# Performance work log

Measured on AMD Instinct MI355X. Metric: run time of the kernel, lower is better.

Reference implementation:

```python
import jax, jax.numpy as jnp
from jax import lax
import numpy as np

B = 2048
N = 10  # wires on q_device0
C64 = jnp.complex64

# fixed gate matrices (qubit ordering matches wire-list order)
S_ = jnp.array([[1, 0], [0, 1j]], C64)
T_ = jnp.array([[1, 0], [0, np.exp(1j * np.pi / 4)]], C64)
SX_ = 0.5 * jnp.array([[1 + 1j, 1 - 1j], [1 - 1j, 1 + 1j]], C64)
Y_ = jnp.array([[0, -1j], [1j, 0]], C64)
CNOT_ = jnp.array([[1, 0, 0, 0], [0, 1, 0, 0], [0, 0, 0, 1], [0, 0, 1, 0]], C64)
CZ_ = jnp.diag(jnp.array([1, 1, 1, -1], C64))
CY_ = jnp.array([[1, 0, 0, 0], [0, 1, 0, 0], [0, 0, 0, -1j], [0, 0, 1j, 0]], C64)
SWAP_ = jnp.array([[1, 0, 0, 0], [0, 0, 1, 0], [0, 1, 0, 0], [0, 0, 0, 1]], C64)
_cs = np.eye(8); _cs[[5, 6]] = _cs[[6, 5]]  # CSWAP: |101> <-> |110>
CSWAP_ = jnp.array(_cs, C64)
_tf = np.eye(8); _tf[[6, 7]] = _tf[[7, 6]]  # Toffoli: |110> <-> |111>
TOFF_ = jnp.array(_tf, C64)

# parametrized single-qubit gate builders; t scalar -> [2,2], t [B] -> [B,2,2]
def _rx(t):
    c = jnp.cos(t / 2).astype(C64)
    s = -1j * jnp.sin(t / 2).astype(C64)
    return jnp.stack([jnp.stack([c, s], -1), jnp.stack([s, c], -1)], -2)

def _ry(t):
    c = jnp.cos(t / 2).astype(C64)
    s = jnp.sin(t / 2).astype(C64)
    return jnp.stack([jnp.stack([c, -s], -1), jnp.stack([s, c], -1)], -2)

def _rz(t):
    a = jnp.exp(-0.5j * t.astype(C64))
    b = jnp.exp(0.5j * t.astype(C64))
    z = jnp.zeros_like(a)
    return jnp.stack([jnp.stack([a, z], -1), jnp.stack([z, b], -1)], -2)

def _phase(t):
    e = jnp.exp(1j * t.astype(C64))
    o = jnp.ones_like(e)
    z = jnp.zeros_like(e)
    return jnp.stack([jnp.stack([o, z], -1), jnp.stack([z, e], -1)], -2)

def _rot(phi, th, om):  # RZ(om) RY(th) RZ(phi), pennylane/torchquantum convention
    c = jnp.cos(th / 2).astype(C64)
    s = jnp.sin(th / 2).astype(C64)
    p = phi.astype(C64); w = om.astype(C64)
    m00 = jnp.exp(-0.5j * (p + w)) * c
    m01 = -jnp.exp(0.5j * (p - w)) * s
    m10 = jnp.exp(-0.5j * (p - w)) * s
    m11 = jnp.exp(0.5j * (p + w)) * c
    return jnp.stack([jnp.stack([m00, m01], -1), jnp.stack([m10, m11], -1)], -2)

def _apply1(psi, U, w):  # psi: [B]+(2,)*N, U: [2,2] or [B,2,2]
    s = jnp.moveaxis(psi, w + 1, 1)
    if U.ndim == 2:
        s = jnp.einsum('ij,bj...->bi...', U, s)
    else:
        s = jnp.einsum('bij,bj...->bi...', U, s)
    return jnp.moveaxis(s, 1, w + 1)

def _applyk(psi, U, wires):  # fixed k-qubit gate, U: [2^k, 2^k]
    k = len(wires)
    axes = tuple(w + 1 for w in wires)
    s = jnp.moveaxis(psi, axes, tuple(range(1, k + 1)))
    sh = s.shape
    s = s.reshape((sh[0], 2 ** k) + sh[k + 1:])
    s = jnp.einsum('ij,bj...->bi...', U, s)
    return jnp.moveaxis(s.reshape(sh), tuple(range(1, k + 1)), axes)

def _forward(x, conv1_w, conv1_b, conv2_w, conv2_b, fc1_w, fc1_b, fc2_w, fc2_b,
             theta0, theta_rz, theta_ps, rot_p):
    dn = ('NCHW', 'OIHW', 'NCHW')
    h = lax.conv_general_dilated(x, conv1_w, (1, 1), 'VALID', dimension_numbers=dn)
    h = jax.nn.relu(h + conv1_b[None, :, None, None])
    h = lax.conv_general_dilated(h, conv2_w, (1, 1), 'VALID', dimension_numbers=dn)
    h = jax.nn.relu(h + conv2_b[None, :, None, None])
    h = lax.reduce_window(h, -jnp.inf, lax.max, (1, 1, 2, 2), (1, 1, 2, 2), 'VALID')
    h = h.reshape(h.shape[0], -1)  # [B, 9216], dropout = identity (eval)
    h = jax.nn.relu(h @ fc1_w.T + fc1_b)
    a = jax.nn.sigmoid(h @ fc2_w.T + fc2_b) * (2.0 * np.pi)  # angles [B, 10]
    bsz = a.shape[0]
    psi = jnp.zeros((bsz, 2 ** N), C64).at[:, 0].set(1.0).reshape((bsz,) + (2,) * N)
    trz = jnp.reshape(theta_rz, ())
    tps = jnp.reshape(theta_ps, ())
    for k in range(N):                      # TrainableRxAll
        psi = _apply1(psi, _rx(theta0[k]), k)
    for k in range(N):                      # RxAll with input angles
        psi = _apply1(psi, _rx(a[:, k]), k)
    psi = _apply1(psi, _rx(a[:, 1]), 1)
    psi = _apply1(psi, _rx(jnp.asarray(-np.pi / 4, jnp.float32)), 5)  # q_layer2 fixed
    psi = _apply1(psi, _ry(a[:, 2]), 2)
    psi = _apply1(psi, _rz(a[:, 3]), 3)
    psi = _apply1(psi, S_, 4)
    psi = _apply1(psi, T_, 5)
    psi = _apply1(psi, _rz(trz), 6)         # q_layer3
    psi = _apply1(psi, SX_, 7)
    # (q_device1 ops on a separate 3-wire device do not affect the output)
    psi = _applyk(psi, CZ_, (0, 5))
    psi = _applyk(psi, CNOT_, (0, 5))
    psi = _applyk(psi, CY_, (0, 5))
    psi = _applyk(psi, CY_, (3, 8))         # q_layer4
    psi = _applyk(psi, SWAP_, (2, 3))
    psi = _applyk(psi, CSWAP_, (4, 5, 6))
    psi = _applyk(psi, TOFF_, (8, 5, 0))    # q_layer5
    psi = _apply1(psi, _phase(tps), 8)      # q_layer6
    psi = _apply1(psi, _phase(a[:, 7]), 7)
    psi = _apply1(psi, _rot(rot_p[0], rot_p[1], rot_p[2]), 4)  # q_layer7
    psi = _apply1(psi, _rot(a[:, 6], a[:, 7], a[:, 8]), 5)
    axes = tuple(range(1, N + 1))
    evs = [jnp.real(jnp.sum(jnp.conj(psi) * _apply1(psi, Y_, k), axis=axes))
           for k in range(N)]
    ev = jnp.stack(evs, -1)                 # [B, 10] <Y_k>
    return jax.nn.log_softmax(ev, axis=1)


def setup_inputs() -> dict:
    key = jax.random.key(0)
    ks = jax.random.split(key, 13)
    return {
        'x': jax.random.normal(ks[0], (B, 1, 28, 28), jnp.float32),
        'conv1_w': jax.random.normal(ks[1], (32, 1, 3, 3), jnp.float32) * 0.2,
        'conv1_b': jnp.zeros((32,), jnp.float32),
        'conv2_w': jax.random.normal(ks[2], (64, 32, 3, 3), jnp.float32) * 0.05,
        'conv2_b': jnp.zeros((64,), jnp.float32),
        'fc1_w': jax.random.normal(ks[3], (128, 9216), jnp.float32) * 0.01,
        'fc1_b': jnp.zeros((128,), jnp.float32),
        'fc2_w': jax.random.normal(ks[4], (10, 128), jnp.float32) * 0.1,
        'fc2_b': jnp.zeros((10,), jnp.float32),
        'theta0': jax.random.normal(ks[5], (10,), jnp.float32),
        'theta_rz': jax.random.normal(ks[6], (1,), jnp.float32),
        'theta_ps': jax.random.normal(ks[7], (1,), jnp.float32),
        'rot_p': jax.random.normal(ks[8], (3,), jnp.float32),
    }


def reference(x, conv1_w, conv1_b, conv2_w, conv2_b, fc1_w, fc1_b, fc2_w, fc2_b,
              theta0, theta_rz, theta_ps, rot_p):
    return _forward(x, conv1_w, conv1_b, conv2_w, conv2_b, fc1_w, fc1_b, fc2_w, fc2_b,
                    theta0, theta_rz, theta_ps, rot_p)
```

## Files before the change

### kernel.cpp

```cpp
#include <hip/hip_runtime.h>
#include <math.h>

typedef short short8 __attribute__((ext_vector_type(8)));
typedef float f32x4 __attribute__((ext_vector_type(4)));
typedef float f32x16 __attribute__((ext_vector_type(16)));

#define GLB_CP(p) ((const __attribute__((address_space(1))) void*)(p))
#define LDS_CP(p) ((__attribute__((address_space(3))) void*)(p))

__device__ __forceinline__ float2 cmul(float2 a, float2 b) {
    return make_float2(a.x * b.x - a.y * b.y, a.x * b.y + a.y * b.x);
}

__device__ __forceinline__ ushort f2bf(float f) {
    uint u = __float_as_uint(f);
    uint r = (u + 0x7FFFu + ((u >> 16) & 1u)) >> 16;
    return (ushort)r;
}

__global__ __launch_bounds__(256) void prep_kernel(
    const float* __restrict__ c2w, const float* __restrict__ f1w,
    ushort* __restrict__ wt2, ushort* __restrict__ wf1)
{
    int i = blockIdx.x * 256 + threadIdx.x;
    if (i < 18432) {
        int icl = i & 7;
        int t = i >> 3;
        int oc = t & 63;
        int t2 = t >> 6;
        int icg = t2 & 3;
        int tap = t2 >> 2;
        int ic = icg * 8 + icl;
        wt2[i] = f2bf(c2w[(oc * 32 + ic) * 9 + tap]);
    } else if (i < 18432 + 1179648) {
        int j = i - 18432;
        wf1[j] = f2bf(f1w[j]);
    }
}

__global__ __launch_bounds__(256) void conv1_kernel(
    const float* __restrict__ x, const float* __restrict__ w1,
    const float* __restrict__ b1, ushort* __restrict__ h1b)
{
    __shared__ float wl[288];
    __shared__ float bl[32];
    int tid = threadIdx.x;
    for (int e = tid; e < 288; e += 256) wl[e] = w1[e];
    if (tid < 32) bl[tid] = b1[tid];
    __syncthreads();
    int e = blockIdx.x * 256 + tid;
    int icg = e & 3;
    int t = e >> 2;
    int pix = t % 676;
    int b = t / 676;
    int y = pix / 26, xc = pix % 26;
    const float* xp = x + b * 784 + y * 28 + xc;
    float in9[9];
#pragma unroll
    for (int ky = 0; ky < 3; ++ky)
#pragma unroll
        for (int kx = 0; kx < 3; ++kx) in9[ky * 3 + kx] = xp[ky * 28 + kx];
    short8 outv;
#pragma unroll
    for (int o = 0; o < 8; ++o) {
        int oc = icg * 8 + o;
        float acc = bl[oc];
#pragma unroll
        for (int k = 0; k < 9; ++k) acc = fmaf(in9[k], wl[oc * 9 + k], acc);
        outv[o] = (short)f2bf(fmaxf(acc, 0.f));
    }
    *(short8*)&h1b[((b * 4 + icg) * 676 + pix) * 8] = outv;
}

__global__ __launch_bounds__(384, 4) void conv2_banded(
    const ushort* __restrict__ h1b, const ushort* __restrict__ wt2,
    const float* __restrict__ c2b, ushort* __restrict__ pooled)
{
    __shared__ __attribute__((aligned(16))) ushort in_lds[8704];
    __shared__ __attribute__((aligned(16))) ushort wt_lds[16384];
    int bx = blockIdx.x;
    int b = bx / 3;
    int band = bx % 3;
    int r0 = band * 8;
    int tid = threadIdx.x;
    int wave = tid >> 6;
    int lane = tid & 63;
    int lo = lane & 31;
    int hi = lane >> 5;

    for (int c = wave; c < 49; c += 6) {
        if (c < 17) {
            int e = c * 64 + lane;
            if (e > 1039) e = 1039;
            int icg = e / 260;
            int rem = e - icg * 260;
            const ushort* src = h1b + ((size_t)(b * 4 + icg) * 676 + r0 * 26 + rem) * 8;
            __builtin_amdgcn_global_load_lds(GLB_CP(src), LDS_CP(in_lds + c * 512), 16, 0, 0);
        } else {
            int e = (c - 17) * 64 + lane;
            const ushort* src = wt2 + e * 8;
            __builtin_amdgcn_global_load_lds(GLB_CP(src), LDS_CP(wt_lds + (c - 17) * 512), 16, 0, 0);
        }
    }

    short8 w8[2][2];
#pragma unroll
    for (int ks = 0; ks < 2; ++ks)
#pragma unroll
        for (int m = 0; m < 2; ++m)
            w8[ks][m] = *(const short8*)(wt2 + (size_t)((32 + ks * 2 + hi) * 64 + m * 32 + lo) * 8);
    float bias0 = c2b[lo];
    float bias1 = c2b[lo + 32];
    __syncthreads();

    int rx = wave % 3, ry = wave / 3;
    int xcoord = rx * 8 + (lo & 7);
    int ycoord = ry * 4 + (lo >> 3);
    int pbase = ycoord * 26 + xcoord;

    f32x16 acc0 = (f32x16)0.f, acc1 = (f32x16)0.f;

#pragma unroll
    for (int tap = 0; tap < 8; ++tap) {
        int off = (tap / 3) * 26 + (tap % 3);
#pragma unroll
        for (int ks = 0; ks < 2; ++ks) {
            short8 bf = *(const short8*)&in_lds[((ks * 2 + hi) * 260 + pbase + off) * 8];
            short8 a0 = *(const short8*)&wt_lds[((tap * 4 + ks * 2 + hi) * 64 + lo) * 8];
            short8 a1 = *(const short8*)&wt_lds[((tap * 4 + ks * 2 + hi) * 64 + 32 + lo) * 8];
            acc0 = __builtin_amdgcn_mfma_f32_32x32x16_bf16(bf, a0, acc0, 0, 0, 0);
            acc1 = __builtin_amdgcn_mfma_f32_32x32x16_bf16(bf, a1, acc1, 0, 0, 0);
        }
    }
    {
        int off = 2 * 26 + 2;
#pragma unroll
        for (int ks = 0; ks < 2; ++ks) {
            short8 bf = *(const short8*)&in_lds[((ks * 2 + hi) * 260 + pbase + off) * 8];
            acc0 = __builtin_amdgcn_mfma_f32_32x32x16_bf16(bf, w8[ks][0], acc0, 0, 0, 0);
            acc1 = __builtin_amdgcn_mfma_f32_32x32x16_bf16(bf, w8[ks][1], acc1, 0, 0, 0);
        }
    }

    ushort* pout = pooled + (size_t)b * 9216;
    int pcolb = rx * 4 + 2 * hi;
#pragma unroll
    for (int q = 0; q < 2; ++q) {
        int prow = band * 4 + ry * 2 + q;
        int base = 8 * q;
        float m00 = fmaxf(fmaxf(acc0[base], acc0[base + 1]), fmaxf(acc0[base + 4], acc0[base + 5]));
        float m01 = fmaxf(fmaxf(acc0[base + 2], acc0[base + 3]), fmaxf(acc0[base + 6], acc0[base + 7]));
        uint pk0 = (uint)f2bf(fmaxf(m00 + bias0, 0.f)) | ((uint)f2bf(fmaxf(m01 + bias0, 0.f)) << 16);
        *(uint*)&pout[lo * 144 + prow * 12 + pcolb] = pk0;
        float m10 = fmaxf(fmaxf(acc1[base], acc1[base + 1]), fmaxf(acc1[base + 4], acc1[base + 5]));
        float m11 = fmaxf(fmaxf(acc1[base + 2], acc1[base + 3]), fmaxf(acc1[base + 6], acc1[base + 7]));
        uint pk1 = (uint)f2bf(fmaxf(m10 + bias1, 0.f)) | ((uint)f2bf(fmaxf(m11 + bias1, 0.f)) << 16);
        *(uint*)&pout[(lo + 32) * 144 + prow * 12 + pcolb] = pk1;
    }
}

__global__ __launch_bounds__(256) void fc1_mfma(
    const ushort* __restrict__ pooled, const ushort* __restrict__ wf1,
    float* __restrict__ part)
{
    int bx = blockIdx.x, by = blockIdx.y;
    int tid = threadIdx.x;
    int wid = tid >> 6, lane = tid & 63;
    int lo = lane & 15, hi = lane >> 4;
    int m0 = bx * 32;
    int kb = by * 2304;

    f32x4 acc[2][2];
#pragma unroll
    for (int mt = 0; mt < 2; ++mt)
#pragma unroll
        for (int j = 0; j < 2; ++j) acc[mt][j] = (f32x4)0.f;

    const ushort* arow0 = pooled + (size_t)(m0 + lo) * 9216 + kb + hi * 8;
    const ushort* arow1 = arow0 + 16 * 9216;
    const ushort* brow0 = wf1 + (size_t)(wid * 32 + lo) * 9216 + kb + hi * 8;
    const ushort* brow1 = brow0 + 16 * 9216;

    for (int kt = 0; kt < 72; ++kt) {
        short8 a0 = *(const short8*)(arow0 + kt * 32);
        short8 a1 = *(const short8*)(arow1 + kt * 32);
        short8 b0 = *(const short8*)(brow0 + kt * 32);
        short8 b1 = *(const short8*)(brow1 + kt * 32);
        acc[0][0] = __builtin_amdgcn_mfma_f32_16x16x32_bf16(a0, b0, acc[0][0], 0, 0, 0);
        acc[1][0] = __builtin_amdgcn_mfma_f32_16x16x32_bf16(a1, b0, acc[1][0], 0, 0, 0);
        acc[0][1] = __builtin_amdgcn_mfma_f32_16x16x32_bf16(a0, b1, acc[0][1], 0, 0, 0);
        acc[1][1] = __builtin_amdgcn_mfma_f32_16x16x32_bf16(a1, b1, acc[1][1], 0, 0, 0);
    }
    float* pp = part + (size_t)by * 262144;
#pragma unroll
    for (int mt = 0; mt < 2; ++mt)
#pragma unroll
        for (int j = 0; j < 2; ++j)
#pragma unroll
            for (int r = 0; r < 4; ++r)
                pp[(m0 + mt * 16 + hi * 4 + r) * 128 + wid * 32 + j * 16 + lo] = acc[mt][j][r];
}

__global__ __launch_bounds__(256) void fc1_reduce_kernel(
    const float* __restrict__ part, const float* __restrict__ bias,
    float* __restrict__ outp)
{
    int idx = blockIdx.x * 256 + threadIdx.x;
    float s = 0.f;
#pragma unroll
    for (int ks = 0; ks < 4; ++ks) s += part[ks * 262144 + idx];
    outp[idx] = fmaxf(s + bias[idx & 127], 0.f);
}

__global__ __launch_bounds__(256) void fc2_kernel(
    const float* __restrict__ h, const float* __restrict__ w,
    const float* __restrict__ bias, float* __restrict__ ang)
{
    int idx = blockIdx.x * 256 + threadIdx.x;
    if (idx >= 20480) return;
    int b = idx / 10, n = idx % 10;
    const float* hp = h + b * 128;
    const float* wp = w + n * 128;
    float s = bias[n];
    for (int k = 0; k < 128; ++k) s = fmaf(hp[k], wp[k], s);
    ang[idx] = 6.28318530718f / (1.f + expf(-s));
}

__device__ __forceinline__ void apply_rot(float2* s, int p, float phi, float th,
                                          float om, int tid)
{
    float c, sn; sincosf(0.5f * th, &sn, &c);
    float A = 0.5f * (phi + om), Bv = 0.5f * (phi - om);
    float cA, sA; sincosf(A, &sA, &cA);
    float cB, sB; sincosf(Bv, &sB, &cB);
    float2 m00 = make_float2(cA * c, -sA * c);
    float2 m01 = make_float2(-cB * sn, -sB * sn);
    float2 m10 = make_float2(cB * sn, -sB * sn);
    float2 m11 = make_float2(cA * c, sA * c);
    for (int q = tid; q < 512; q += 256) {
        int i0 = ((q >> p) << (p + 1)) | (q & ((1 << p) - 1));
        int i1 = i0 | (1 << p);
        float2 aa = s[i0], bb = s[i1];
        s[i0] = make_float2(m00.x * aa.x - m00.y * aa.y + m01.x * bb.x - m01.y * bb.y,
                            m00.x * aa.y + m00.y * aa.x + m01.x * bb.y + m01.y * bb.x);
        s[i1] = make_float2(m10.x * aa.x - m10.y * aa.y + m11.x * bb.x - m11.y * bb.y,
                            m10.x * aa.y + m10.y * aa.x + m11.x * bb.y + m11.y * bb.x);
    }
}

__global__ __launch_bounds__(256) void quantum_kernel(
    const float* __restrict__ ang, const float* __restrict__ theta0,
    const float* __restrict__ theta_rz, const float* __restrict__ theta_ps,
    const float* __restrict__ rot_p, float* __restrict__ out)
{
    __shared__ float2 s[1024];
    __shared__ float red[40];
    int b = blockIdx.x;
    int tid = threadIdx.x;

    float a[10];
#pragma unroll
    for (int k = 0; k < 10; ++k) a[k] = ang[b * 10 + k];
    float th[10];
#pragma unroll
    for (int k = 0; k < 10; ++k) th[k] = theta0[k] + a[k];
    th[1] += a[1];
    th[5] -= 0.78539816339745f;

    float2 v[10][2];
#pragma unroll
    for (int k = 0; k < 10; ++k) {
        float c, sn; sincosf(0.5f * th[k], &sn, &c);
        v[k][0] = make_float2(c, 0.f);
        v[k][1] = make_float2(0.f, -sn);
    }
    { float c, sn; sincosf(0.5f * a[2], &sn, &c);
      float2 v0 = v[2][0], v1 = v[2][1];
      v[2][0] = make_float2(c * v0.x - sn * v1.x, c * v0.y - sn * v1.y);
      v[2][1] = make_float2(sn * v0.x + c * v1.x, sn * v0.y + c * v1.y); }
    { float c, sn; sincosf(0.5f * a[3], &sn, &c);
      v[3][0] = cmul(v[3][0], make_float2(c, -sn));
      v[3][1] = cmul(v[3][1], make_float2(c, sn)); }
    { float2 t = v[4][1]; v[4][1] = make_float2(-t.y, t.x); }
    { const float r = 0.70710678118655f;
      float2 t = v[5][1]; v[5][1] = make_float2(r * (t.x - t.y), r * (t.x + t.y)); }
    { float c, sn; sincosf(0.5f * theta_rz[0], &sn, &c);
      v[6][0] = cmul(v[6][0], make_float2(c, -sn));
      v[6][1] = cmul(v[6][1], make_float2(c, sn)); }
    { float2 p = v[7][0], q = v[7][1];
      v[7][0] = make_float2(0.5f * ((p.x - p.y) + (q.x + q.y)),
                            0.5f * ((p.x + p.y) + (q.y - q.x)));
      v[7][1] = make_float2(0.5f * ((p.x + p.y) + (q.x - q.y)),
                            0.5f * ((p.y - p.x) + (q.x + q.y))); }

    for (int i = tid; i < 1024; i += 256) {
        float2 c = ((i >> 9) & 1) ? v[0][1] : v[0][0];
#pragma unroll
        for (int k = 1; k < 10; ++k) {
            float2 vk = ((i >> (9 - k)) & 1) ? v[k][1] : v[k][0];
            c = cmul(c, vk);
        }
        s[i] = c;
    }
    __syncthreads();

    for (int i = tid; i < 1024; i += 256)
        if (((i >> 9) & 1) && ((i >> 4) & 1)) { s[i].x = -s[i].x; s[i].y = -s[i].y; }
    __syncthreads();
    { int j = tid;
      int i0 = 512 | ((j >> 4) << 5) | (j & 15);
      int i1 = i0 | 16;
      float2 t0 = s[i0], t1 = s[i1];
      s[i0] = t1; s[i1] = t0; }
    __syncthreads();
    { int j = tid;
      int i0 = 512 | ((j >> 4) << 5) | (j & 15);
      int i1 = i0 | 16;
      float2 t0 = s[i0], t1 = s[i1];
      s[i0] = make_float2(t1.y, -t1.x);
      s[i1] = make_float2(-t0.y, t0.x); }
    __syncthreads();
    { int j = tid;
      int i0 = (j & 1) | (((j >> 1) & 15) << 2) | (((j >> 5) & 7) << 7) | 64;
      int i1 = i0 | 2;
      float2 t0 = s[i0], t1 = s[i1];
      s[i0] = make_float2(t1.y, -t1.x);
      s[i1] = make_float2(-t0.y, t0.x); }
    __syncthreads();
    { int j = tid;
      int i0 = (j & 63) | 128 | (((j >> 6) & 3) << 8);
      int i1 = i0 ^ 0xC0;
      float2 t0 = s[i0], t1 = s[i1];
      s[i0] = t1; s[i1] = t0; }
    __syncthreads();
    if (tid < 128) {
      int j = tid;
      int i0 = (j & 7) | 16 | 32 | (((j >> 3) & 15) << 6);
      int i1 = i0 ^ 0x18;
      float2 t0 = s[i0], t1 = s[i1];
      s[i0] = t1; s[i1] = t0; }
    __syncthreads();
    if (tid < 128) {
      int j = tid;
      int i0 = (j & 1) | 2 | (((j >> 1) & 3) << 2) | 16 | (((j >> 3) & 15) << 5);
      int i1 = i0 | 512;
      float2 t0 = s[i0], t1 = s[i1];
      s[i0] = t1; s[i1] = t0; }
    __syncthreads();
    { float c1, s1; sincosf(theta_ps[0], &s1, &c1);
      float c2, s2; sincosf(a[7], &s2, &c2);
      float2 p1 = make_float2(c1, s1), p2 = make_float2(c2, s2);
      for (int i = tid; i < 1024; i += 256) {
          float2 t = s[i];
          if ((i >> 1) & 1) t = cmul(t, p1);
          if ((i >> 2) & 1) t = cmul(t, p2);
          s[i] = t;
      } }
    __syncthreads();
    apply_rot(s, 5, rot_p[0], rot_p[1], rot_p[2], tid);
    __syncthreads();
    apply_rot(s, 4, a[6], a[7], a[8], tid);
    __syncthreads();

    int wave = tid >> 6;
    for (int k = 0; k < 10; ++k) {
        int p = 9 - k;
        float part = 0.f;
        for (int q = tid; q < 512; q += 256) {
            int i0 = ((q >> p) << (p + 1)) | (q & ((1 << p) - 1));
            int i1 = i0 | (1 << p);
            float2 aa = s[i0], bb = s[i1];
            part += aa.x * bb.y - aa.y * bb.x;
        }
        part *= 2.f;
#pragma unroll
        for (int off = 32; off > 0; off >>= 1)
            part += __shfl_down(part, off, 64);
        if ((tid & 63) == 0) red[k * 4 + wave] = part;
    }
    __syncthreads();
    if (tid == 0) {
        float ev[10];
        float mx = -1e30f;
#pragma unroll
        for (int k = 0; k < 10; ++k) {
            ev[k] = red[k * 4] + red[k * 4 + 1] + red[k * 4 + 2] + red[k * 4 + 3];
            mx = fmaxf(mx, ev[k]);
        }
        float sum = 0.f;
#pragma unroll
        for (int k = 0; k < 10; ++k) sum += expf(ev[k] - mx);
        float lse = mx + logf(sum);
#pragma unroll
        for (int k = 0; k < 10; ++k) out[b * 10 + k] = ev[k] - lse;
    }
}

extern "C" void kernel_launch(void* const* d_in, const int* in_sizes, int n_in,
                              void* d_out, int out_size, void* d_ws, size_t ws_size,
                              hipStream_t stream)
{
    (void)in_sizes; (void)n_in; (void)out_size; (void)ws_size;
    const float* x    = (const float*)d_in[0];
    const float* c1w  = (const float*)d_in[1];
    const float* c1b  = (const float*)d_in[2];
    const float* c2w  = (const float*)d_in[3];
    const float* c2b  = (const float*)d_in[4];
    const float* f1w  = (const float*)d_in[5];
    const float* f1b  = (const float*)d_in[6];
    const float* f2w  = (const float*)d_in[7];
    const float* f2b  = (const float*)d_in[8];
    const float* th0  = (const float*)d_in[9];
    const float* trz  = (const float*)d_in[10];
    const float* tps  = (const float*)d_in[11];
    const float* rotp = (const float*)d_in[12];
    float* out = (float*)d_out;

    char* ws = (char*)d_ws;
    ushort* h1b    = (ushort*)(ws);
    ushort* pooled = (ushort*)(ws + 88604672);
    ushort* wt2    = (ushort*)(ws + 126353408);
    ushort* wf1    = (ushort*)(ws + 126390272);
    float*  part   = (float*)(ws + 128749568);
    float*  fc1o   = (float*)(ws + 132943872);
    float*  ang    = (float*)(ws + 133992448);

    prep_kernel<<<4680, 256, 0, stream>>>(c2w, f1w, wt2, wf1);
    conv1_kernel<<<21632, 256, 0, stream>>>(x, c1w, c1b, h1b);
    conv2_banded<<<6144, 384, 0, stream>>>(h1b, wt2, c2b, pooled);
    fc1_mfma<<<dim3(64, 4), 256, 0, stream>>>(pooled, wf1, part);
    fc1_reduce_kernel<<<1024, 256, 0, stream>>>(part, f1b, fc1o);
    fc2_kernel<<<80, 256, 0, stream>>>(fc1o, f2w, f2b, ang);
    quantum_kernel<<<2048, 256, 0, stream>>>(ang, th0, trz, tps, rotp, out);
}
```

Baseline: 165.8 us.

## Process whole image per conv2 block with double-buffered band prefetch

Result: faster. 161.0 us (-2.9%).

```diff
diff --git a/kernel.cpp b/kernel.cpp
--- a/kernel.cpp
+++ b/kernel.cpp
@@ -72,43 +72,34 @@
     *(short8*)&h1b[((b * 4 + icg) * 676 + pix) * 8] = outv;
 }
 
-__global__ __launch_bounds__(384, 4) void conv2_banded(
+__global__ __launch_bounds__(384, 3) void conv2_img(
     const ushort* __restrict__ h1b, const ushort* __restrict__ wt2,
     const float* __restrict__ c2b, ushort* __restrict__ pooled)
 {
-    __shared__ __attribute__((aligned(16))) ushort in_lds[8704];
-    __shared__ __attribute__((aligned(16))) ushort wt_lds[16384];
-    int bx = blockIdx.x;
-    int b = bx / 3;
-    int band = bx % 3;
-    int r0 = band * 8;
+    __shared__ __attribute__((aligned(16))) ushort wt_lds[18432];
+    __shared__ __attribute__((aligned(16))) ushort in_lds[2][8704];
+    int b = blockIdx.x;
     int tid = threadIdx.x;
     int wave = tid >> 6;
     int lane = tid & 63;
     int lo = lane & 31;
     int hi = lane >> 5;
 
-    for (int c = wave; c < 49; c += 6) {
-        if (c < 17) {
+    for (int c = wave; c < 36; c += 6) {
+        const ushort* src = wt2 + (size_t)(c * 64 + lane) * 8;
+        __builtin_amdgcn_global_load_lds(GLB_CP(src), LDS_CP(wt_lds + c * 512), 16, 0, 0);
+    }
+    {
+        const ushort* base = h1b + (size_t)b * 21632;
+        for (int c = wave; c < 17; c += 6) {
             int e = c * 64 + lane;
             if (e > 1039) e = 1039;
             int icg = e / 260;
             int rem = e - icg * 260;
-            const ushort* src = h1b + ((size_t)(b * 4 + icg) * 676 + r0 * 26 + rem) * 8;
-            __builtin_amdgcn_global_load_lds(GLB_CP(src), LDS_CP(in_lds + c * 512), 16, 0, 0);
-        } else {
-            int e = (c - 17) * 64 + lane;
-            const ushort* src = wt2 + e * 8;
-            __builtin_amdgcn_global_load_lds(GLB_CP(src), LDS_CP(wt_lds + (c - 17) * 512), 16, 0, 0);
-        }
-    }
-
-    short8 w8[2][2];
-#pragma unroll
-    for (int ks = 0; ks < 2; ++ks)
-#pragma unroll
-        for (int m = 0; m < 2; ++m)
-            w8[ks][m] = *(const short8*)(wt2 + (size_t)((32 + ks * 2 + hi) * 64 + m * 32 + lo) * 8);
+            const ushort* src = base + ((size_t)icg * 676 + rem) * 8;
+            __builtin_amdgcn_global_load_lds(GLB_CP(src), LDS_CP(in_lds[0] + c * 512), 16, 0, 0);
+        }
+    }
     float bias0 = c2b[lo];
     float bias1 = c2b[lo + 32];
     __syncthreads();
@@ -117,45 +108,53 @@
     int xcoord = rx * 8 + (lo & 7);
     int ycoord = ry * 4 + (lo >> 3);
     int pbase = ycoord * 26 + xcoord;
-
-    f32x16 acc0 = (f32x16)0.f, acc1 = (f32x16)0.f;
-
-#pragma unroll
-    for (int tap = 0; tap < 8; ++tap) {
-        int off = (tap / 3) * 26 + (tap % 3);
-#pragma unroll
-        for (int ks = 0; ks < 2; ++ks) {
-            short8 bf = *(const short8*)&in_lds[((ks * 2 + hi) * 260 + pbase + off) * 8];
-            short8 a0 = *(const short8*)&wt_lds[((tap * 4 + ks * 2 + hi) * 64 + lo) * 8];
-            short8 a1 = *(const short8*)&wt_lds[((tap * 4 + ks * 2 + hi) * 64 + 32 + lo) * 8];
-            acc0 = __builtin_amdgcn_mfma_f32_32x32x16_bf16(bf, a0, acc0, 0, 0, 0);
-            acc1 = __builtin_amdgcn_mfma_f32_32x32x16_bf16(bf, a1, acc1, 0, 0, 0);
-        }
-    }
-    {
-        int off = 2 * 26 + 2;
-#pragma unroll
-        for (int ks = 0; ks < 2; ++ks) {
-            short8 bf = *(const short8*)&in_lds[((ks * 2 + hi) * 260 + pbase + off) * 8];
-            acc0 = __builtin_amdgcn_mfma_f32_32x32x16_bf16(bf, w8[ks][0], acc0, 0, 0, 0);
-            acc1 = __builtin_amdgcn_mfma_f32_32x32x16_bf16(bf, w8[ks][1], acc1, 0, 0, 0);
-        }
-    }
-
     ushort* pout = pooled + (size_t)b * 9216;
     int pcolb = rx * 4 + 2 * hi;
-#pragma unroll
-    for (int q = 0; q < 2; ++q) {
-        int prow = band * 4 + ry * 2 + q;
-        int base = 8 * q;
-        float m00 = fmaxf(fmaxf(acc0[base], acc0[base + 1]), fmaxf(acc0[base + 4], acc0[base + 5]));
-        float m01 = fmaxf(fmaxf(acc0[base + 2], acc0[base + 3]), fmaxf(acc0[base + 6], acc0[base + 7]));
-        uint pk0 = (uint)f2bf(fmaxf(m00 + bias0, 0.f)) | ((uint)f2bf(fmaxf(m01 + bias0, 0.f)) << 16);
-        *(uint*)&pout[lo * 144 + prow * 12 + pcolb] = pk0;
-        float m10 = fmaxf(fmaxf(acc1[base], acc1[base + 1]), fmaxf(acc1[base + 4], acc1[base + 5]));
-        float m11 = fmaxf(fmaxf(acc1[base + 2], acc1[base + 3]), fmaxf(acc1[base + 6], acc1[base + 7]));
-        uint pk1 = (uint)f2bf(fmaxf(m10 + bias1, 0.f)) | ((uint)f2bf(fmaxf(m11 + bias1, 0.f)) << 16);
-        *(uint*)&pout[(lo + 32) * 144 + prow * 12 + pcolb] = pk1;
+
+#pragma unroll
+    for (int band = 0; band < 3; ++band) {
+        if (band < 2) {
+            const ushort* base = h1b + (size_t)b * 21632 + (size_t)(band + 1) * 8 * 26 * 8;
+            ushort* dst = in_lds[(band + 1) & 1];
+            for (int c = wave; c < 17; c += 6) {
+                int e = c * 64 + lane;
+                if (e > 1039) e = 1039;
+                int icg = e / 260;
+                int rem = e - icg * 260;
+                const ushort* src = base + ((size_t)icg * 676 + rem) * 8;
+                __builtin_amdgcn_global_load_lds(GLB_CP(src), LDS_CP(dst + c * 512), 16, 0, 0);
+            }
+        }
+
+        const ushort* ib = in_lds[band & 1];
+        f32x16 acc0 = (f32x16)0.f, acc1 = (f32x16)0.f;
+#pragma unroll
+        for (int tap = 0; tap < 9; ++tap) {
+            int off = (tap / 3) * 26 + (tap % 3);
+#pragma unroll
+            for (int ks = 0; ks < 2; ++ks) {
+                short8 bf = *(const short8*)&ib[((ks * 2 + hi) * 260 + pbase + off) * 8];
+                short8 a0 = *(const short8*)&wt_lds[((tap * 4 + ks * 2 + hi) * 64 + lo) * 8];
+                short8 a1 = *(const short8*)&wt_lds[((tap * 4 + ks * 2 + hi) * 64 + 32 + lo) * 8];
+                acc0 = __builtin_amdgcn_mfma_f32_32x32x16_bf16(bf, a0, acc0, 0, 0, 0);
+                acc1 = __builtin_amdgcn_mfma_f32_32x32x16_bf16(bf, a1, acc1, 0, 0, 0);
+            }
+        }
+
+#pragma unroll
+        for (int q = 0; q < 2; ++q) {
+            int prow = band * 4 + ry * 2 + q;
+            int base = 8 * q;
+            float m00 = fmaxf(fmaxf(acc0[base], acc0[base + 1]), fmaxf(acc0[base + 4], acc0[base + 5]));
+            float m01 = fmaxf(fmaxf(acc0[base + 2], acc0[base + 3]), fmaxf(acc0[base + 6], acc0[base + 7]));
+            uint pk0 = (uint)f2bf(fmaxf(m00 + bias0, 0.f)) | ((uint)f2bf(fmaxf(m01 + bias0, 0.f)) << 16);
+            *(uint*)&pout[lo * 144 + prow * 12 + pcolb] = pk0;
+            float m10 = fmaxf(fmaxf(acc1[base], acc1[base + 1]), fmaxf(acc1[base + 4], acc1[base + 5]));
+            float m11 = fmaxf(fmaxf(acc1[base + 2], acc1[base + 3]), fmaxf(acc1[base + 6], acc1[base + 7]));
+            uint pk1 = (uint)f2bf(fmaxf(m10 + bias1, 0.f)) | ((uint)f2bf(fmaxf(m11 + bias1, 0.f)) << 16);
+            *(uint*)&pout[(lo + 32) * 144 + prow * 12 + pcolb] = pk1;
+        }
+        __syncthreads();
     }
 }
 
@@ -427,7 +426,7 @@
 
     prep_kernel<<<4680, 256, 0, stream>>>(c2w, f1w, wt2, wf1);
     conv1_kernel<<<21632, 256, 0, stream>>>(x, c1w, c1b, h1b);
-    conv2_banded<<<6144, 384, 0, stream>>>(h1b, wt2, c2b, pooled);
+    conv2_img<<<2048, 384, 0, stream>>>(h1b, wt2, c2b, pooled);
     fc1_mfma<<<dim3(64, 4), 256, 0, stream>>>(pooled, wf1, part);
     fc1_reduce_kernel<<<1024, 256, 0, stream>>>(part, f1b, fc1o);
     fc2_kernel<<<80, 256, 0, stream>>>(fc1o, f2w, f2b, ang);
```
